# Optimization experiments

Hardware: AMD Instinct MI355X
Metric: run time of the kernel (lower is better)

## Reference

```python
import jax, jax.numpy as jnp
import numpy as np

KERNEL = 8
STRIDE = 4
K_LIST = [KERNEL // 2, KERNEL, KERNEL + KERNEL // 2]  # [4, 8, 12]


def _unfold(x, k, s):
    # x: (N, C, H, W) -> (N, L, C, k, k), windows row-major (h outer, w inner)
    N, C, H, W = x.shape
    oh = (H - k) // s + 1
    ow = (W - k) // s + 1
    rows = (jnp.arange(oh) * s)[:, None] + jnp.arange(k)  # (oh, k)
    cols = (jnp.arange(ow) * s)[:, None] + jnp.arange(k)  # (ow, k)
    # advanced indexing broadcast -> (N, C, oh, ow, k, k)
    p = x[:, :, rows[:, None, :, None], cols[None, :, None, :]]
    return p.transpose(0, 2, 3, 1, 4, 5).reshape(N, oh * ow, C, k, k)


def _adaptive_avg_mat(n_in, n_out):
    # PyTorch adaptive_avg_pool1d bin edges: [floor(i*n_in/n_out), ceil((i+1)*n_in/n_out))
    M = np.zeros((n_out, n_in), dtype=np.float32)
    for i in range(n_out):
        s = (i * n_in) // n_out
        e = -((-(i + 1) * n_in) // n_out)
        M[i, s:e] = 1.0 / (e - s)
    return jnp.asarray(M)


def setup_inputs() -> dict:
    key = jax.random.key(0)
    k1, k2, k3 = jax.random.split(key, 3)
    x = jax.random.normal(k1, (8, 64, 256, 256), dtype=jnp.float32)
    w_reduce = jax.random.normal(k2, (16, 64), dtype=jnp.float32) / np.sqrt(64.0)
    b_reduce = jax.random.normal(k3, (16,), dtype=jnp.float32) * 0.01
    return {"x": x, "w_reduce": w_reduce, "b_reduce": b_reduce}


def reference(x, w_reduce, b_reduce):
    N, C, H, W = x.shape
    # crop to even H, W
    x = x[:, :, : H - (H % 2), : W - (W % 2)]
    # replicate pad by 1 on each side
    x = jnp.pad(x, ((0, 0), (0, 0), (1, 1), (1, 1)), mode="edge")
    # 1x1 conv reduce: C -> C // 4
    x = jnp.einsum("nchw,oc->nohw", x, w_reduce) + b_reduce[None, :, None, None]

    outs = []
    for k in K_LIST:
        p = _unfold(x, k, STRIDE)  # (N, L, Cr, k, k)
        Nn, L, Cr = p.shape[:3]
        if k < KERNEL:
            # bilinear upsample (align_corners=False, half-pixel centers)
            p = jax.image.resize(
                p.reshape(Nn * L, Cr, k, k),
                (Nn * L, Cr, KERNEL, KERNEL),
                method="bilinear",
            ).reshape(Nn, L, Cr, KERNEL, KERNEL)
        elif k > KERNEL:
            M = _adaptive_avg_mat(k, KERNEL)  # (KERNEL, k)
            p = jnp.einsum("nlcij,pi,qj->nlcpq", p, M, M)
        outs.append(p)
    # concat along the window dimension
    return jnp.concatenate(outs, axis=1)  # (N, 11909, Cr, 8, 8)
```

## Files before the change

### kernel.cpp

```cpp
#include <hip/hip_runtime.h>

#define C_IN 64
#define C_OUT 16
#define H 256
#define W 256
#define HW 65536
#define N_B 8
#define L4 4096
#define L8 3969
#define L12 3844
#define LTOT 11909
#define LDSP 260

typedef float f4v __attribute__((ext_vector_type(4)));
typedef unsigned short us4a __attribute__((ext_vector_type(4), aligned(2)));

__device__ __forceinline__ void nt_store4(const float4& v, float* p) {
  f4v t; t.x = v.x; t.y = v.y; t.z = v.z; t.w = v.w;
  __builtin_nontemporal_store(t, reinterpret_cast<f4v*>(p));
}

__device__ __forceinline__ unsigned short f2b(float f) {
  union { float f; unsigned u; } v; v.f = f;
  const unsigned r = v.u + 0x7FFFu + ((v.u >> 16) & 1u);
  return (unsigned short)(r >> 16);
}
__device__ __forceinline__ float b2f(unsigned short h) {
  union { unsigned u; float f; } v; v.u = ((unsigned)h) << 16;
  return v.f;
}

__device__ __forceinline__ float4 load4cb(const unsigned short* __restrict__ row, int ws0) {
  if (ws0 >= 0) {
    us4a t = *reinterpret_cast<const us4a*>(row + ws0);
    return make_float4(b2f(t.x), b2f(t.y), b2f(t.z), b2f(t.w));
  }
  return make_float4(b2f(row[0]), b2f(row[0]), b2f(row[1]), b2f(row[2]));
}

__global__ __launch_bounds__(256) void reduce_kernel(
    const float* __restrict__ x, const float* __restrict__ w,
    const float* __restrict__ b, unsigned short* __restrict__ y) {
  __shared__ float wt[C_IN][C_OUT];
  for (int i = threadIdx.x; i < C_IN * C_OUT; i += 256)
    wt[i & 63][i >> 6] = w[i];
  __syncthreads();

  const unsigned gid = blockIdx.x * 256 + threadIdx.x;
  const int n = gid >> 14;
  const int pix = (gid & 16383) << 2;
  const float* xp = x + (size_t)n * C_IN * HW + pix;

  float4 acc[C_OUT];
#pragma unroll
  for (int o = 0; o < C_OUT; ++o) {
    const float bv = b[o];
    acc[o] = make_float4(bv, bv, bv, bv);
  }

#define FMA4(A, WS) \
  A.x = fmaf(xv.x, WS, A.x); A.y = fmaf(xv.y, WS, A.y); \
  A.z = fmaf(xv.z, WS, A.z); A.w = fmaf(xv.w, WS, A.w);

#pragma unroll
  for (int c = 0; c < C_IN; ++c) {
    const float4 xv = *reinterpret_cast<const float4*>(xp + (size_t)c * HW);
    const float4 w0 = *reinterpret_cast<const float4*>(&wt[c][0]);
    const float4 w1 = *reinterpret_cast<const float4*>(&wt[c][4]);
    const float4 w2 = *reinterpret_cast<const float4*>(&wt[c][8]);
    const float4 w3 = *reinterpret_cast<const float4*>(&wt[c][12]);
    FMA4(acc[0], w0.x)  FMA4(acc[1], w0.y)  FMA4(acc[2], w0.z)  FMA4(acc[3], w0.w)
    FMA4(acc[4], w1.x)  FMA4(acc[5], w1.y)  FMA4(acc[6], w1.z)  FMA4(acc[7], w1.w)
    FMA4(acc[8], w2.x)  FMA4(acc[9], w2.y)  FMA4(acc[10], w2.z) FMA4(acc[11], w2.w)
    FMA4(acc[12], w3.x) FMA4(acc[13], w3.y) FMA4(acc[14], w3.z) FMA4(acc[15], w3.w)
  }
#undef FMA4

  unsigned short* yp = y + (size_t)n * C_OUT * HW + pix;
#pragma unroll
  for (int o = 0; o < C_OUT; ++o) {
    us4a t;
    t.x = f2b(acc[o].x); t.y = f2b(acc[o].y);
    t.z = f2b(acc[o].z); t.w = f2b(acc[o].w);
    *reinterpret_cast<us4a*>(yp + (size_t)o * HW) = t;
  }
}

__global__ __launch_bounds__(256) void patch_fused_kernel(
    const unsigned short* __restrict__ y, float* __restrict__ out) {
  const int CP = 12 * LDSP + 8;
  __shared__ float lds[4 * (12 * LDSP + 8)];
  const int bid = blockIdx.x;
  const int oh = bid & 63;
  const int cq = (bid >> 6) & 3;
  const int n = bid >> 8;
  const int tid = threadIdx.x;

#pragma unroll
  for (int i = 0; i < 12; ++i) {
    const int sid = i * 256 + tid;
    const int c = sid / 768;
    const int rem = sid - c * 768;
    const int t = rem >> 6;
    const int k = rem & 63;
    const int r = min(max(oh * 4 + t - 1, 0), H - 1);
    const float4 v = load4cb(y + (size_t)(n * C_OUT + cq * 4 + c) * HW + (size_t)r * W, 4 * k - 1);
    *reinterpret_cast<float4*>(&lds[c * CP + t * LDSP + 4 * k]) = v;
  }
  __syncthreads();

  const int lane = tid & 63;
  const int c = lane >> 4;
  const int p = (lane >> 1) & 7;
  const int qh = lane & 1;
  const int lrow = tid >> 6;
  const float* lc = &lds[c * CP];
  const size_t obase = ((size_t)n * LTOT) * (C_OUT * 64) + (size_t)(cq * 4 + c) * 64 + p * 8 + qh * 4;

  {
    const int ip0 = max(0, (p - 1) >> 1), ip1 = min(3, (p + 1) >> 1);
    const float wp0 = (p == 0 || p == 7) ? 1.0f : ((p & 1) ? 0.75f : 0.25f);
    const float wp1 = 1.0f - wp0;
    const float* lr0 = lc + ip0 * LDSP;
    const float* lr1 = lc + ip1 * LDSP;
    float* ob = out + obase + (size_t)(oh * 64) * (C_OUT * 64);

#pragma unroll
    for (int i = 0; i < 16; ++i) {
      const int ow = i * 4 + lrow;
      const float4 A = *reinterpret_cast<const float4*>(lr0 + ow * 4);
      const float4 B = *reinterpret_cast<const float4*>(lr1 + ow * 4);
      float4 ta, tb;
      if (qh == 0) {
        ta = make_float4(A.x, 0.75f * A.x + 0.25f * A.y, 0.25f * A.x + 0.75f * A.y, 0.75f * A.y + 0.25f * A.z);
        tb = make_float4(B.x, 0.75f * B.x + 0.25f * B.y, 0.25f * B.x + 0.75f * B.y, 0.75f * B.y + 0.25f * B.z);
      } else {
        ta = make_float4(0.25f * A.y + 0.75f * A.z, 0.75f * A.z + 0.25f * A.w, 0.25f * A.z + 0.75f * A.w, A.w);
        tb = make_float4(0.25f * B.y + 0.75f * B.z, 0.75f * B.z + 0.25f * B.w, 0.25f * B.z + 0.75f * B.w, B.w);
      }
      const float4 v = make_float4(wp0 * ta.x + wp1 * tb.x, wp0 * ta.y + wp1 * tb.y,
                                   wp0 * ta.z + wp1 * tb.z, wp0 * ta.w + wp1 * tb.w);
      nt_store4(v, ob + (size_t)ow * (C_OUT * 64));
    }
  }

  if (oh < 63) {
    const float* lr = lc + p * LDSP + qh * 4;
    float* ob = out + obase + (size_t)(L4 + oh * 63) * (C_OUT * 64);
#pragma unroll
    for (int i = 0; i < 16; ++i) {
      const int ow = i * 4 + lrow;
      if (ow < 63) {
        const float4 v = *reinterpret_cast<const float4*>(lr + ow * 4);
        nt_store4(v, ob + (size_t)ow * (C_OUT * 64));
      }
    }
  }

  if (oh < 62) {
    const int a = (3 * p) >> 1;
    const float* r0 = lc + a * LDSP;
    const float* r1 = r0 + LDSP;
    float* ob = out + obase + (size_t)(L4 + L8 + oh * 62) * (C_OUT * 64);
#pragma unroll
    for (int i = 0; i < 16; ++i) {
      const int ow = i * 4 + lrow;
      if (ow < 62) {
        const float4 F40 = *reinterpret_cast<const float4*>(r0 + ow * 4 + qh * 8);
        const float2 F20 = *reinterpret_cast<const float2*>(r0 + ow * 4 + 4 + qh * 2);
        const float4 F41 = *reinterpret_cast<const float4*>(r1 + ow * 4 + qh * 8);
        const float2 F21 = *reinterpret_cast<const float2*>(r1 + ow * 4 + 4 + qh * 2);
        const float e0 = qh ? F20.x : F40.x, f0 = qh ? F21.x : F41.x;
        const float e1 = qh ? F20.y : F40.y, f1 = qh ? F21.y : F41.y;
        const float e2 = qh ? F40.x : F40.z, f2 = qh ? F41.x : F41.z;
        const float e3 = qh ? F40.y : F40.w, f3 = qh ? F41.y : F41.w;
        const float e4 = qh ? F40.z : F20.x, f4 = qh ? F41.z : F21.x;
        const float e5 = qh ? F40.w : F20.y, f5 = qh ? F41.w : F21.y;
        const float4 v = make_float4(0.25f * (e0 + e1 + f0 + f1),
                                     0.25f * (e1 + e2 + f1 + f2),
                                     0.25f * (e3 + e4 + f3 + f4),
                                     0.25f * (e4 + e5 + f4 + f5));
        nt_store4(v, ob + (size_t)ow * (C_OUT * 64));
      }
    }
  }
}

extern "C" void kernel_launch(void* const* d_in, const int* in_sizes, int n_in,
                              void* d_out, int out_size, void* d_ws, size_t ws_size,
                              hipStream_t stream) {
  const float* x = (const float*)d_in[0];
  const float* w = (const float*)d_in[1];
  const float* b = (const float*)d_in[2];
  float* out = (float*)d_out;
  unsigned short* y = (unsigned short*)d_ws;

  reduce_kernel<<<512, 256, 0, stream>>>(x, w, b, y);
  patch_fused_kernel<<<N_B * 4 * 64, 256, 0, stream>>>(y, out);
}
```

Baseline: 108.5 us.

## Tile patch kernel over two output rows and two channels with aligned bf16 loads

Each patch block now covers two output window rows for two channels, loading 16 input rows into LDS instead of 12 rows for one window row. This lowers the redundant row reloads caused by overlapping windows. Global loads become aligned 8-element bf16 vectors with the replicate-pad column written separately, replacing misaligned 4-element loads and their edge branch. The store mapping changes so each wave covers two windows with two channels each, which alters write contiguity on the dominant output stream.

New measurement: 107.4 us, median of 2. No clear change (-1.0%).

```diff
diff --git a/kernel.cpp b/kernel.cpp
--- a/kernel.cpp
+++ b/kernel.cpp
@@ -13,7 +13,8 @@
 #define LDSP 260
 
 typedef float f4v __attribute__((ext_vector_type(4)));
-typedef unsigned short us4a __attribute__((ext_vector_type(4), aligned(2)));
+typedef unsigned short us8 __attribute__((ext_vector_type(8)));
+typedef unsigned short us4 __attribute__((ext_vector_type(4)));
 
 __device__ __forceinline__ void nt_store4(const float4& v, float* p) {
   f4v t; t.x = v.x; t.y = v.y; t.z = v.z; t.w = v.w;
@@ -28,14 +29,6 @@
 __device__ __forceinline__ float b2f(unsigned short h) {
   union { unsigned u; float f; } v; v.u = ((unsigned)h) << 16;
   return v.f;
-}
-
-__device__ __forceinline__ float4 load4cb(const unsigned short* __restrict__ row, int ws0) {
-  if (ws0 >= 0) {
-    us4a t = *reinterpret_cast<const us4a*>(row + ws0);
-    return make_float4(b2f(t.x), b2f(t.y), b2f(t.z), b2f(t.w));
-  }
-  return make_float4(b2f(row[0]), b2f(row[0]), b2f(row[1]), b2f(row[2]));
 }
 
 __global__ __launch_bounds__(256) void reduce_kernel(
@@ -79,108 +72,118 @@
   unsigned short* yp = y + (size_t)n * C_OUT * HW + pix;
 #pragma unroll
   for (int o = 0; o < C_OUT; ++o) {
-    us4a t;
+    us4 t;
     t.x = f2b(acc[o].x); t.y = f2b(acc[o].y);
     t.z = f2b(acc[o].z); t.w = f2b(acc[o].w);
-    *reinterpret_cast<us4a*>(yp + (size_t)o * HW) = t;
+    *reinterpret_cast<us4*>(yp + (size_t)o * HW) = t;
   }
 }
 
 __global__ __launch_bounds__(256) void patch_fused_kernel(
     const unsigned short* __restrict__ y, float* __restrict__ out) {
-  const int CP = 12 * LDSP + 8;
-  __shared__ float lds[4 * (12 * LDSP + 8)];
+  const int CP = 16 * LDSP + 8;
+  __shared__ float lds[2 * (16 * LDSP + 8)];
   const int bid = blockIdx.x;
-  const int oh = bid & 63;
-  const int cq = (bid >> 6) & 3;
-  const int n = bid >> 8;
+  const int j  = bid & 31;
+  const int cp = (bid >> 5) & 7;
+  const int n  = bid >> 8;
   const int tid = threadIdx.x;
 
 #pragma unroll
-  for (int i = 0; i < 12; ++i) {
-    const int sid = i * 256 + tid;
-    const int c = sid / 768;
-    const int rem = sid - c * 768;
-    const int t = rem >> 6;
-    const int k = rem & 63;
-    const int r = min(max(oh * 4 + t - 1, 0), H - 1);
-    const float4 v = load4cb(y + (size_t)(n * C_OUT + cq * 4 + c) * HW + (size_t)r * W, 4 * k - 1);
-    *reinterpret_cast<float4*>(&lds[c * CP + t * LDSP + 4 * k]) = v;
+  for (int pass = 0; pass < 4; ++pass) {
+    const int sid = pass * 256 + tid;
+    const int c  = sid >> 9;
+    const int tp = (sid >> 5) & 15;
+    const int ch = sid & 31;
+    const int r = min(max(8 * j + tp - 1, 0), H - 1);
+    const us8 v = *reinterpret_cast<const us8*>(
+        y + (size_t)(n * C_OUT + cp * 2 + c) * HW + (size_t)r * W + ch * 8);
+    float* d = &lds[c * CP + tp * LDSP + ch * 8 + 1];
+#pragma unroll
+    for (int e = 0; e < 8; ++e) d[e] = b2f(v[e]);
+    if (ch == 0) d[-1] = b2f(v.x);
   }
   __syncthreads();
 
   const int lane = tid & 63;
-  const int c = lane >> 4;
-  const int p = (lane >> 1) & 7;
+  const int z  = lane >> 5;
+  const int c  = (lane >> 4) & 1;
+  const int p  = (lane >> 1) & 7;
   const int qh = lane & 1;
   const int lrow = tid >> 6;
   const float* lc = &lds[c * CP];
-  const size_t obase = ((size_t)n * LTOT) * (C_OUT * 64) + (size_t)(cq * 4 + c) * 64 + p * 8 + qh * 4;
-
-  {
-    const int ip0 = max(0, (p - 1) >> 1), ip1 = min(3, (p + 1) >> 1);
-    const float wp0 = (p == 0 || p == 7) ? 1.0f : ((p & 1) ? 0.75f : 0.25f);
-    const float wp1 = 1.0f - wp0;
-    const float* lr0 = lc + ip0 * LDSP;
-    const float* lr1 = lc + ip1 * LDSP;
-    float* ob = out + obase + (size_t)(oh * 64) * (C_OUT * 64);
-
-#pragma unroll
-    for (int i = 0; i < 16; ++i) {
-      const int ow = i * 4 + lrow;
-      const float4 A = *reinterpret_cast<const float4*>(lr0 + ow * 4);
-      const float4 B = *reinterpret_cast<const float4*>(lr1 + ow * 4);
-      float4 ta, tb;
-      if (qh == 0) {
-        ta = make_float4(A.x, 0.75f * A.x + 0.25f * A.y, 0.25f * A.x + 0.75f * A.y, 0.75f * A.y + 0.25f * A.z);
-        tb = make_float4(B.x, 0.75f * B.x + 0.25f * B.y, 0.25f * B.x + 0.75f * B.y, 0.75f * B.y + 0.25f * B.z);
-      } else {
-        ta = make_float4(0.25f * A.y + 0.75f * A.z, 0.75f * A.z + 0.25f * A.w, 0.25f * A.z + 0.75f * A.w, A.w);
-        tb = make_float4(0.25f * B.y + 0.75f * B.z, 0.75f * B.z + 0.25f * B.w, 0.25f * B.z + 0.75f * B.w, B.w);
-      }
-      const float4 v = make_float4(wp0 * ta.x + wp1 * tb.x, wp0 * ta.y + wp1 * tb.y,
-                                   wp0 * ta.z + wp1 * tb.z, wp0 * ta.w + wp1 * tb.w);
-      nt_store4(v, ob + (size_t)ow * (C_OUT * 64));
-    }
-  }
-
-  if (oh < 63) {
-    const float* lr = lc + p * LDSP + qh * 4;
-    float* ob = out + obase + (size_t)(L4 + oh * 63) * (C_OUT * 64);
-#pragma unroll
-    for (int i = 0; i < 16; ++i) {
-      const int ow = i * 4 + lrow;
-      if (ow < 63) {
-        const float4 v = *reinterpret_cast<const float4*>(lr + ow * 4);
+  const size_t obase0 = ((size_t)n * LTOT) * (C_OUT * 64)
+                        + (size_t)(cp * 2 + c) * 64 + p * 8 + qh * 4;
+
+#pragma unroll
+  for (int sub = 0; sub < 2; ++sub) {
+    const int oh = 2 * j + sub;
+    const int rb = sub * 4;
+
+    {
+      const int ip0 = max(0, (p - 1) >> 1), ip1 = min(3, (p + 1) >> 1);
+      const float wp0 = (p == 0 || p == 7) ? 1.0f : ((p & 1) ? 0.75f : 0.25f);
+      const float wp1 = 1.0f - wp0;
+      const float* lr0 = lc + (rb + ip0) * LDSP;
+      const float* lr1 = lc + (rb + ip1) * LDSP;
+      float* ob = out + obase0 + (size_t)(oh * 64) * (C_OUT * 64);
+#pragma unroll
+      for (int i = 0; i < 8; ++i) {
+        const int ow = i * 8 + lrow * 2 + z;
+        const float4 A = *reinterpret_cast<const float4*>(lr0 + ow * 4);
+        const float4 B = *reinterpret_cast<const float4*>(lr1 + ow * 4);
+        float4 ta, tb;
+        if (qh == 0) {
+          ta = make_float4(A.x, 0.75f * A.x + 0.25f * A.y, 0.25f * A.x + 0.75f * A.y, 0.75f * A.y + 0.25f * A.z);
+          tb = make_float4(B.x, 0.75f * B.x + 0.25f * B.y, 0.25f * B.x + 0.75f * B.y, 0.75f * B.y + 0.25f * B.z);
+        } else {
+          ta = make_float4(0.25f * A.y + 0.75f * A.z, 0.75f * A.z + 0.25f * A.w, 0.25f * A.z + 0.75f * A.w, A.w);
+          tb = make_float4(0.25f * B.y + 0.75f * B.z, 0.75f * B.z + 0.25f * B.w, 0.25f * B.z + 0.75f * B.w, B.w);
+        }
+        const float4 v = make_float4(wp0 * ta.x + wp1 * tb.x, wp0 * ta.y + wp1 * tb.y,
+                                     wp0 * ta.z + wp1 * tb.z, wp0 * ta.w + wp1 * tb.w);
         nt_store4(v, ob + (size_t)ow * (C_OUT * 64));
       }
     }
-  }
-
-  if (oh < 62) {
-    const int a = (3 * p) >> 1;
-    const float* r0 = lc + a * LDSP;
-    const float* r1 = r0 + LDSP;
-    float* ob = out + obase + (size_t)(L4 + L8 + oh * 62) * (C_OUT * 64);
-#pragma unroll
-    for (int i = 0; i < 16; ++i) {
-      const int ow = i * 4 + lrow;
-      if (ow < 62) {
-        const float4 F40 = *reinterpret_cast<const float4*>(r0 + ow * 4 + qh * 8);
-        const float2 F20 = *reinterpret_cast<const float2*>(r0 + ow * 4 + 4 + qh * 2);
-        const float4 F41 = *reinterpret_cast<const float4*>(r1 + ow * 4 + qh * 8);
-        const float2 F21 = *reinterpret_cast<const float2*>(r1 + ow * 4 + 4 + qh * 2);
-        const float e0 = qh ? F20.x : F40.x, f0 = qh ? F21.x : F41.x;
-        const float e1 = qh ? F20.y : F40.y, f1 = qh ? F21.y : F41.y;
-        const float e2 = qh ? F40.x : F40.z, f2 = qh ? F41.x : F41.z;
-        const float e3 = qh ? F40.y : F40.w, f3 = qh ? F41.y : F41.w;
-        const float e4 = qh ? F40.z : F20.x, f4 = qh ? F41.z : F21.x;
-        const float e5 = qh ? F40.w : F20.y, f5 = qh ? F41.w : F21.y;
-        const float4 v = make_float4(0.25f * (e0 + e1 + f0 + f1),
-                                     0.25f * (e1 + e2 + f1 + f2),
-                                     0.25f * (e3 + e4 + f3 + f4),
-                                     0.25f * (e4 + e5 + f4 + f5));
-        nt_store4(v, ob + (size_t)ow * (C_OUT * 64));
+
+    if (oh < 63) {
+      const float* lr = lc + (rb + p) * LDSP + qh * 4;
+      float* ob = out + obase0 + (size_t)(L4 + oh * 63) * (C_OUT * 64);
+#pragma unroll
+      for (int i = 0; i < 8; ++i) {
+        const int ow = i * 8 + lrow * 2 + z;
+        if (ow < 63) {
+          const float4 v = *reinterpret_cast<const float4*>(lr + ow * 4);
+          nt_store4(v, ob + (size_t)ow * (C_OUT * 64));
+        }
+      }
+    }
+
+    if (oh < 62) {
+      const int a = (3 * p) >> 1;
+      const float* r0 = lc + (rb + a) * LDSP;
+      const float* r1 = r0 + LDSP;
+      float* ob = out + obase0 + (size_t)(L4 + L8 + oh * 62) * (C_OUT * 64);
+#pragma unroll
+      for (int i = 0; i < 8; ++i) {
+        const int ow = i * 8 + lrow * 2 + z;
+        if (ow < 62) {
+          const float4 F40 = *reinterpret_cast<const float4*>(r0 + ow * 4 + qh * 8);
+          const float2 F20 = *reinterpret_cast<const float2*>(r0 + ow * 4 + 4 + qh * 2);
+          const float4 F41 = *reinterpret_cast<const float4*>(r1 + ow * 4 + qh * 8);
+          const float2 F21 = *reinterpret_cast<const float2*>(r1 + ow * 4 + 4 + qh * 2);
+          const float e0 = qh ? F20.x : F40.x, f0 = qh ? F21.x : F41.x;
+          const float e1 = qh ? F20.y : F40.y, f1 = qh ? F21.y : F41.y;
+          const float e2 = qh ? F40.x : F40.z, f2 = qh ? F41.x : F41.z;
+          const float e3 = qh ? F40.y : F40.w, f3 = qh ? F41.y : F41.w;
+          const float e4 = qh ? F40.z : F20.x, f4 = qh ? F41.z : F21.x;
+          const float e5 = qh ? F40.w : F20.y, f5 = qh ? F41.w : F21.y;
+          const float4 v = make_float4(0.25f * (e0 + e1 + f0 + f1),
+                                       0.25f * (e1 + e2 + f1 + f2),
+                                       0.25f * (e3 + e4 + f3 + f4),
+                                       0.25f * (e4 + e5 + f4 + f5));
+          nt_store4(v, ob + (size_t)ow * (C_OUT * 64));
+        }
       }
     }
   }
@@ -196,5 +199,5 @@
   unsigned short* y = (unsigned short*)d_ws;
 
   reduce_kernel<<<512, 256, 0, stream>>>(x, w, b, y);
-  patch_fused_kernel<<<N_B * 4 * 64, 256, 0, stream>>>(y, out);
-}
+  patch_fused_kernel<<<N_B * 8 * 32, 256, 0, stream>>>(y, out);
+}
```
